# Performance work log

Measured on AMD Instinct MI355X. Metric: run time of the kernel, lower is better.

The kernel has to match this reference:

```python
import jax, jax.numpy as jnp
import numpy as np
import math

N_USER = 50000
N_ITEM = 50000
E_PER = 400000
F_IN = 128
F_OUT = 128
H = 4
D = F_OUT // H  # 32
NUM_ET = 2  # edge types: 0 = user->item, 1 = item->user


def setup_inputs() -> dict:
    key = jax.random.key(0)
    ks = jax.random.split(key, 16)
    s = 0.05  # weight scale to keep activations tame
    return {
        "x_user": jax.random.normal(ks[0], (N_USER, F_IN), jnp.float32),
        "x_item": jax.random.normal(ks[1], (N_ITEM, F_IN), jnp.float32),
        "W_kqv_user": jax.random.normal(ks[2], (F_IN, 3 * F_OUT), jnp.float32) * s,
        "b_kqv_user": jax.random.normal(ks[3], (3 * F_OUT,), jnp.float32) * s,
        "W_kqv_item": jax.random.normal(ks[4], (F_IN, 3 * F_OUT), jnp.float32) * s,
        "b_kqv_item": jax.random.normal(ks[5], (3 * F_OUT,), jnp.float32) * s,
        "Wk_rel": jax.random.normal(ks[6], (H * NUM_ET, D, D), jnp.float32) * s,
        "Wv_rel": jax.random.normal(ks[7], (H * NUM_ET, D, D), jnp.float32) * s,
        "W_out_user": jax.random.normal(ks[8], (F_OUT, F_OUT), jnp.float32) * s,
        "b_out_user": jax.random.normal(ks[9], (F_OUT,), jnp.float32) * s,
        "W_out_item": jax.random.normal(ks[10], (F_OUT, F_OUT), jnp.float32) * s,
        "b_out_item": jax.random.normal(ks[11], (F_OUT,), jnp.float32) * s,
        "skip_user": jnp.ones((1,), jnp.float32),
        "skip_item": jnp.ones((1,), jnp.float32),
        "p_rel_ui": jnp.ones((H,), jnp.float32),
        "p_rel_iu": jnp.ones((H,), jnp.float32),
        "edge_ui": jax.random.randint(ks[12], (2, E_PER), 0, N_USER, dtype=jnp.int32),
        "edge_iu": jax.random.randint(ks[13], (2, E_PER), 0, N_ITEM, dtype=jnp.int32),
    }


def _kqv(x, W, b):
    o = x @ W + b  # [N, 3F]
    k, q, v = o[:, :F_OUT], o[:, F_OUT:2 * F_OUT], o[:, 2 * F_OUT:]
    return (k.reshape(-1, H, D), q.reshape(-1, H, D), v.reshape(-1, H, D))


def _rel(x, Wrel, et):
    # HeteroLinear with type index h*NUM_ET + et per head (is_sorted layout)
    W = Wrel[jnp.arange(H) * NUM_ET + et]  # [H, D, D]
    return jnp.einsum('nhd,hde->nhe', x, W)


def reference(x_user, x_item, W_kqv_user, b_kqv_user, W_kqv_item, b_kqv_item,
              Wk_rel, Wv_rel, W_out_user, b_out_user, W_out_item, b_out_item,
              skip_user, skip_item, p_rel_ui, p_rel_iu, edge_ui, edge_iu):
    ku, qu, vu = _kqv(x_user, W_kqv_user, b_kqv_user)
    ki, qi, vi = _kqv(x_item, W_kqv_item, b_kqv_item)

    # per-edge-type relation transform of K/V (grouped GEMM by head x edge-type)
    k0, v0 = _rel(ku, Wk_rel, 0), _rel(vu, Wv_rel, 0)  # src of user->item
    k1, v1 = _rel(ki, Wk_rel, 1), _rel(vi, Wv_rel, 1)  # src of item->user

    q_all = jnp.concatenate([qu, qi], 0)  # dst offsets: user=0, item=N_USER
    n_tot = N_USER + N_ITEM

    src0, dst0 = edge_ui[0], edge_ui[1] + N_USER
    src1, dst1 = edge_iu[0], edge_iu[1]

    kj = jnp.concatenate([k0[src0], k1[src1]], 0)  # [E, H, D]
    vj = jnp.concatenate([v0[src0], v1[src1]], 0)  # [E, H, D]
    dst = jnp.concatenate([dst0, dst1], 0)         # [E]
    p = jnp.concatenate([jnp.broadcast_to(p_rel_ui, (E_PER, H)),
                         jnp.broadcast_to(p_rel_iu, (E_PER, H))], 0)

    qe = q_all[dst]                                  # [E, H, D]
    alpha = (qe * kj).sum(-1) * p / math.sqrt(D)     # [E, H]

    # segment softmax over destination nodes (PyG softmax: max-shift, +1e-16)
    amax = jax.ops.segment_max(alpha, dst, num_segments=n_tot)
    a = jnp.exp(alpha - amax[dst])
    denom = jax.ops.segment_sum(a, dst, num_segments=n_tot)
    a = a / (denom[dst] + 1e-16)

    out = jax.ops.segment_sum(vj * a[:, :, None], dst, num_segments=n_tot)
    out = out.reshape(n_tot, F_OUT)
    out_u, out_i = out[:N_USER], out[N_USER:]

    g = lambda t: jax.nn.gelu(t, approximate=False)
    a_u = g(out_u) @ W_out_user + b_out_user
    a_i = g(out_i) @ W_out_item + b_out_item

    su = jax.nn.sigmoid(skip_user)  # out_channels == in_channels -> skip blend
    si = jax.nn.sigmoid(skip_item)
    return (su * a_u + (1.0 - su) * x_user,
            si * a_i + (1.0 - si) * x_item)
```

## Files before the change

### kernel.cpp

```cpp
#include <hip/hip_runtime.h>
#include <hip/hip_bf16.h>
#include <math.h>

#define N_USERS 50000
#define N_ITEMS 50000
#define NN      100000
#define E_PER_  400000
#define E_TOT   800000
#define FDIM    128
#define NH      4
#define HD      32
#define SCAN_CHUNK 1024
#define SCAN_NB    ((NN + SCAN_CHUNK - 1) / SCAN_CHUNK)
#define KQV_NB  ((N_USERS + 127) / 128)

typedef __attribute__((ext_vector_type(8))) short bfrag;
typedef __attribute__((ext_vector_type(4))) float f32x4;

__device__ __forceinline__ float gelu_exact(float x) {
    return 0.5f * x * (1.0f + erff(x * 0.70710678118654752f));
}
__device__ __forceinline__ unsigned short f2bf(float f) {
    unsigned u = __float_as_uint(f);
    unsigned r = u + 0x7fffu + ((u >> 16) & 1u);
    return (unsigned short)(r >> 16);
}
__device__ __forceinline__ void unpack8(uint4 u, float* f) {
    f[0] = __uint_as_float(u.x << 16); f[1] = __uint_as_float(u.x & 0xffff0000u);
    f[2] = __uint_as_float(u.y << 16); f[3] = __uint_as_float(u.y & 0xffff0000u);
    f[4] = __uint_as_float(u.z << 16); f[5] = __uint_as_float(u.z & 0xffff0000u);
    f[6] = __uint_as_float(u.w << 16); f[7] = __uint_as_float(u.w & 0xffff0000u);
}
__device__ __forceinline__ size_t wfrag_idx(int n, int k) {
    int ch = n >> 7, nt = (n >> 4) & 7, lr = n & 15;
    int ks = k >> 5, lg = (k >> 3) & 3, e = k & 7;
    return ((size_t)(((ch * 8 + nt) * 4 + ks) * 64 + lg * 16 + lr)) * 8 + e;
}

__global__ void prep_kqv(
    const float* __restrict__ W_u, const float* __restrict__ b_u,
    const float* __restrict__ W_i, const float* __restrict__ b_i,
    const float* __restrict__ Wk_rel, const float* __restrict__ Wv_rel,
    unsigned short* __restrict__ F_u, float* __restrict__ bias_u,
    unsigned short* __restrict__ F_i, float* __restrict__ bias_i)
{
    const int et = blockIdx.x >= 384;
    const int n = blockIdx.x - et * 384;
    const int k = threadIdx.x;
    const float* W = et ? W_i : W_u;
    const float* b = et ? b_i : b_u;
    unsigned short* F = et ? F_i : F_u;
    float* bias_f = et ? bias_i : bias_u;
    float s;
    if (n < 128) {
        int h = n >> 5, e = n & 31;
        const float* wr = Wk_rel + (size_t)(h * 2 + et) * 1024 + e;
        const float* wc = W + (size_t)k * 384 + h * 32;
        s = 0.f;
        for (int d = 0; d < 32; ++d) s = fmaf(wc[d], wr[d * 32], s);
        if (k == 0) {
            float bs = 0.f;
            for (int d = 0; d < 32; ++d) bs = fmaf(b[h * 32 + d], wr[d * 32], bs);
            bias_f[n] = bs;
        }
    } else if (n < 256) {
        s = W[(size_t)k * 384 + n];
        if (k == 0) bias_f[n] = b[n];
    } else {
        int h = (n - 256) >> 5, e = (n - 256) & 31;
        const float* wr = Wv_rel + (size_t)(h * 2 + et) * 1024 + e;
        const float* wc = W + (size_t)k * 384 + 256 + h * 32;
        s = 0.f;
        for (int d = 0; d < 32; ++d) s = fmaf(wc[d], wr[d * 32], s);
        if (k == 0) {
            float bs = 0.f;
            for (int d = 0; d < 32; ++d) bs = fmaf(b[256 + h * 32 + d], wr[d * 32], bs);
            bias_f[n] = bs;
        }
    }
    F[wfrag_idx(n, k)] = f2bf(s);
}

__global__ void prep_wo(
    const float* __restrict__ W_u, unsigned short* __restrict__ F_u,
    const float* __restrict__ W_i, unsigned short* __restrict__ F_i)
{
    int i = blockIdx.x * blockDim.x + threadIdx.x;
    int side = i >= 128 * 128;
    int j = i - side * 128 * 128;
    if (j >= 128 * 128) return;
    int n = j >> 7, k = j & 127;
    const float* W = side ? W_i : W_u;
    unsigned short* F = side ? F_i : F_u;
    F[wfrag_idx(n, k)] = f2bf(W[(size_t)k * 128 + n]);
}

__global__ __launch_bounds__(256, 3) void kqv_mfma(
    const float* __restrict__ X_u, const unsigned short* __restrict__ F_u,
    const float* __restrict__ bias_u,
    const float* __restrict__ X_i, const unsigned short* __restrict__ F_i,
    const float* __restrict__ bias_i,
    unsigned short* __restrict__ kk_b,
    unsigned short* __restrict__ q_b,
    unsigned short* __restrict__ vv_b)
{
    const int t = threadIdx.x;
    const int side = blockIdx.x >= KQV_NB;
    const int m0 = (blockIdx.x - side * KQV_NB) * 128;
    const float* X = side ? X_i : X_u;
    const unsigned short* F = side ? F_i : F_u;
    const float* bias = side ? bias_i : bias_u;
    const int side_off = side ? N_USERS : 0;
    const int M = N_USERS;

    const int wave = t >> 6, lane = t & 63;
    const int lr = lane & 15, lg = lane >> 4;
    const int rbase = m0 + wave * 32;

    bfrag am[2][4];
    #pragma unroll
    for (int mt = 0; mt < 2; ++mt)
        #pragma unroll
        for (int ks = 0; ks < 4; ++ks) {
            int row = rbase + mt * 16 + lr;
            float4 a = make_float4(0.f, 0.f, 0.f, 0.f);
            float4 b4 = make_float4(0.f, 0.f, 0.f, 0.f);
            if (row < M) {
                const float* px = X + (size_t)row * 128 + ks * 32 + lg * 8;
                a  = *reinterpret_cast<const float4*>(px);
                b4 = *reinterpret_cast<const float4*>(px + 4);
            }
            uint4 pk;
            pk.x = (unsigned)f2bf(a.x)  | ((unsigned)f2bf(a.y)  << 16);
            pk.y = (unsigned)f2bf(a.z)  | ((unsigned)f2bf(a.w)  << 16);
            pk.z = (unsigned)f2bf(b4.x) | ((unsigned)f2bf(b4.y) << 16);
            pk.w = (unsigned)f2bf(b4.z) | ((unsigned)f2bf(b4.w) << 16);
            am[mt][ks] = *reinterpret_cast<bfrag*>(&pk);
        }

    #pragma unroll
    for (int ch = 0; ch < 3; ++ch) {
        f32x4 acc[2][8];
        const f32x4 zero = {0.f, 0.f, 0.f, 0.f};
        #pragma unroll
        for (int mt = 0; mt < 2; ++mt)
            #pragma unroll
            for (int nt = 0; nt < 8; ++nt) acc[mt][nt] = zero;

        bfrag bc[4], bn[4];
        #pragma unroll
        for (int ks = 0; ks < 4; ++ks)
            bc[ks] = *reinterpret_cast<const bfrag*>(
                F + ((size_t)((ch * 8 + 0) * 4 + ks) * 64 + lane) * 8);

        #pragma unroll
        for (int nt = 0; nt < 8; ++nt) {
            if (nt < 7) {
                #pragma unroll
                for (int ks = 0; ks < 4; ++ks)
                    bn[ks] = *reinterpret_cast<const bfrag*>(
                        F + ((size_t)((ch * 8 + nt + 1) * 4 + ks) * 64 + lane) * 8);
            }
            #pragma unroll
            for (int mt = 0; mt < 2; ++mt)
                #pragma unroll
                for (int ks = 0; ks < 4; ++ks)
                    acc[mt][nt] = __builtin_amdgcn_mfma_f32_16x16x32_bf16(
                        bc[ks], am[mt][ks], acc[mt][nt], 0, 0, 0);
            #pragma unroll
            for (int ks = 0; ks < 4; ++ks) bc[ks] = bn[ks];
        }

        unsigned short* arr = (ch == 0) ? kk_b : (ch == 1) ? q_b : vv_b;
        #pragma unroll
        for (int nt = 0; nt < 8; ++nt) {
            float4 bv = *reinterpret_cast<const float4*>(bias + ch * 128 + nt * 16 + lg * 4);
            #pragma unroll
            for (int mt = 0; mt < 2; ++mt) {
                int row = rbase + mt * 16 + lr;
                if (row < M) {
                    unsigned lo = (unsigned)f2bf(acc[mt][nt][0] + bv.x)
                                | ((unsigned)f2bf(acc[mt][nt][1] + bv.y) << 16);
                    unsigned hi = (unsigned)f2bf(acc[mt][nt][2] + bv.z)
                                | ((unsigned)f2bf(acc[mt][nt][3] + bv.w) << 16);
                    uint2 st = make_uint2(lo, hi);
                    *reinterpret_cast<uint2*>(
                        arr + (size_t)(side_off + row) * 128 + nt * 16 + lg * 4) = st;
                }
            }
        }
    }
}

__device__ __forceinline__ void edge_src_dst(
    int e, const int* __restrict__ edge_ui, const int* __restrict__ edge_iu,
    int& src, int& dst)
{
    if (e < E_PER_) {
        src = edge_ui[e];
        dst = edge_ui[E_PER_ + e] + N_USERS;
    } else {
        int e2 = e - E_PER_;
        src = N_USERS + edge_iu[e2];
        dst = edge_iu[E_PER_ + e2];
    }
}

__global__ __launch_bounds__(256) void hist_kernel(
    const int* __restrict__ edge_ui, const int* __restrict__ edge_iu,
    int* __restrict__ cnt)
{
    int e = blockIdx.x * blockDim.x + threadIdx.x;
    if (e >= E_TOT) return;
    int src, dst;
    edge_src_dst(e, edge_ui, edge_iu, src, dst);
    atomicAdd(cnt + dst, 1);
}

__global__ __launch_bounds__(256) void scan1_kernel(
    const int* __restrict__ cnt, int* __restrict__ base, int* __restrict__ bsum)
{
    __shared__ int ssum[256];
    const int t = threadIdx.x;
    const int i0 = blockIdx.x * SCAN_CHUNK + t * 4;
    int v[4];
    #pragma unroll
    for (int j = 0; j < 4; ++j) v[j] = (i0 + j < NN) ? cnt[i0 + j] : 0;
    int tsum = v[0] + v[1] + v[2] + v[3];
    ssum[t] = tsum;
    __syncthreads();
    int run = tsum;
    for (int off = 1; off < 256; off <<= 1) {
        int o = (t >= off) ? ssum[t - off] : 0;
        __syncthreads();
        run += o;
        ssum[t] = run;
        __syncthreads();
    }
    int excl = run - tsum;
    int p = excl;
    #pragma unroll
    for (int j = 0; j < 4; ++j) {
        if (i0 + j < NN) base[i0 + j] = p;
        p += v[j];
    }
    if (t == 255) bsum[blockIdx.x] = run;
}

__global__ __launch_bounds__(256) void scan3_kernel(
    int* __restrict__ base, const int* __restrict__ bsum, int* __restrict__ cursor)
{
    const int lane = threadIdx.x & 63;
    const int chunk = blockIdx.x >> 2;
    int v0 = (lane < chunk) ? bsum[lane] : 0;
    int v1 = (64 + lane < chunk && 64 + lane < SCAN_NB) ? bsum[64 + lane] : 0;
    int s = v0 + v1;
    #pragma unroll
    for (int off = 1; off < 64; off <<= 1) s += __shfl_xor(s, off);
    int i = blockIdx.x * 256 + threadIdx.x;
    if (i < NN) {
        int b = base[i] + s;
        base[i] = b;
        cursor[i] = b;
    }
}

__global__ __launch_bounds__(256) void fill_kernel(
    const int* __restrict__ edge_ui, const int* __restrict__ edge_iu,
    int* __restrict__ cursor, int* __restrict__ esrc)
{
    int e = blockIdx.x * blockDim.x + threadIdx.x;
    if (e >= E_TOT) return;
    int src, dst;
    edge_src_dst(e, edge_ui, edge_iu, src, dst);
    int pos = atomicAdd(cursor + dst, 1);
    esrc[pos] = src;
}

__global__ __launch_bounds__(256) void attn_fused(
    const unsigned short* __restrict__ q_b, const unsigned short* __restrict__ kk_b,
    const unsigned short* __restrict__ vv_b,
    const int* __restrict__ base, const int* __restrict__ cnt,
    const int* __restrict__ esrc,
    const float* __restrict__ p_ui, const float* __restrict__ p_iu,
    unsigned short* __restrict__ oa)
{
    const int wid  = (blockIdx.x * blockDim.x + threadIdx.x) >> 6;
    const int lane = threadIdx.x & 63;
    const int nw   = (gridDim.x * blockDim.x) >> 6;
    const int g    = lane >> 3;
    const int p    = lane & 7;
    const int h    = p >> 1;
    const float rsd = 0.17677669529663687f;
    const float pu = p_ui[h], pi = p_iu[h];

    for (int n = wid; n < NN; n += nw) {
        const float pr = (n >= N_USERS) ? pu : pi;
        float qf[16];
        {
            const unsigned short* qrow = q_b + (size_t)n * 128 + p * 16;
            unpack8(*reinterpret_cast<const uint4*>(qrow), qf);
            unpack8(*reinterpret_cast<const uint4*>(qrow + 8), qf + 8);
        }
        float l = 0.f;
        float acc[16];
        #pragma unroll
        for (int i = 0; i < 16; ++i) acc[i] = 0.f;
        const int s0 = base[n], c = cnt[n];

        for (int j = 0; j < c; j += 8) {
            int jj = j + g;
            bool valid = jj < c;
            int src = esrc[s0 + (valid ? jj : 0)];
            const unsigned short* krow = kk_b + (size_t)src * 128 + p * 16;
            const unsigned short* vrow = vv_b + (size_t)src * 128 + p * 16;
            uint4 k4a = *reinterpret_cast<const uint4*>(krow);
            uint4 k4b = *reinterpret_cast<const uint4*>(krow + 8);
            uint4 v4a = *reinterpret_cast<const uint4*>(vrow);
            uint4 v4b = *reinterpret_cast<const uint4*>(vrow + 8);
            float kf[16];
            unpack8(k4a, kf); unpack8(k4b, kf + 8);
            float s = qf[0] * kf[0];
            #pragma unroll
            for (int i = 1; i < 16; ++i) s = fmaf(qf[i], kf[i], s);
            s += __shfl_xor(s, 1);
            float w = valid ? __expf(s * pr * rsd) : 0.f;
            l += w;
            float vf[16];
            unpack8(v4a, vf); unpack8(v4b, vf + 8);
            #pragma unroll
            for (int i = 0; i < 16; ++i) acc[i] = fmaf(w, vf[i], acc[i]);
        }

        l += __shfl_xor(l, 8); l += __shfl_xor(l, 16); l += __shfl_xor(l, 32);

        const bool b2 = (g & 4) != 0;
        float k8[8];
        #pragma unroll
        for (int i = 0; i < 8; ++i) {
            float mine = b2 ? acc[8 + i] : acc[i];
            float send = b2 ? acc[i] : acc[8 + i];
            k8[i] = mine + __shfl_xor(send, 32);
        }
        const bool b1 = (g & 2) != 0;
        float k4r[4];
        #pragma unroll
        for (int i = 0; i < 4; ++i) {
            float mine = b1 ? k8[4 + i] : k8[i];
            float send = b1 ? k8[i] : k8[4 + i];
            k4r[i] = mine + __shfl_xor(send, 16);
        }
        const bool b0 = (g & 1) != 0;
        float k2[2];
        #pragma unroll
        for (int i = 0; i < 2; ++i) {
            float mine = b0 ? k4r[2 + i] : k4r[i];
            float send = b0 ? k4r[i] : k4r[2 + i];
            k2[i] = mine + __shfl_xor(send, 8);
        }
        float inv = 1.0f / (l + 1e-16f);
        unsigned pk = (unsigned)f2bf(gelu_exact(k2[0] * inv))
                    | ((unsigned)f2bf(gelu_exact(k2[1] * inv)) << 16);
        *reinterpret_cast<unsigned*>(oa + (size_t)n * 128 + p * 16 + 2 * g) = pk;
    }
}

__global__ __launch_bounds__(256, 3) void final_mfma(
    const unsigned short* __restrict__ oa,
    const float* __restrict__ x_u, const unsigned short* __restrict__ F_u,
    const float* __restrict__ bo_u, const float* __restrict__ skip_u,
    const float* __restrict__ x_i, const unsigned short* __restrict__ F_i,
    const float* __restrict__ bo_i, const float* __restrict__ skip_i,
    float* __restrict__ out)
{
    const int t = threadIdx.x;
    const int side = blockIdx.x >= KQV_NB;
    const int m0 = (blockIdx.x - side * KQV_NB) * 128;
    const float* x = side ? x_i : x_u;
    const unsigned short* F = side ? F_i : F_u;
    const float* bo = side ? bo_i : bo_u;
    const float* skip = side ? skip_i : skip_u;
    const int row_off = side ? N_USERS : 0;
    const int M = N_USERS;

    const int wave = t >> 6, lane = t & 63;
    const int lr = lane & 15, lg = lane >> 4;
    const int rbase = m0 + wave * 32;

    bfrag am[2][4];
    const bfrag bz = {0, 0, 0, 0, 0, 0, 0, 0};
    #pragma unroll
    for (int mt = 0; mt < 2; ++mt)
        #pragma unroll
        for (int ks = 0; ks < 4; ++ks) {
            int row = rbase + mt * 16 + lr;
            am[mt][ks] = (row < M)
                ? *reinterpret_cast<const bfrag*>(
                      oa + (size_t)(row_off + row) * 128 + ks * 32 + lg * 8)
                : bz;
        }

    f32x4 acc[2][8];
    const f32x4 zero = {0.f, 0.f, 0.f, 0.f};
    #pragma unroll
    for (int mt = 0; mt < 2; ++mt)
        #pragma unroll
        for (int nt = 0; nt < 8; ++nt) acc[mt][nt] = zero;

    bfrag bc[4], bn[4];
    #pragma unroll
    for (int ks = 0; ks < 4; ++ks)
        bc[ks] = *reinterpret_cast<const bfrag*>(
            F + ((size_t)(0 * 4 + ks) * 64 + lane) * 8);

    #pragma unroll
    for (int nt = 0; nt < 8; ++nt) {
        if (nt < 7) {
            #pragma unroll
            for (int ks = 0; ks < 4; ++ks)
                bn[ks] = *reinterpret_cast<const bfrag*>(
                    F + ((size_t)((nt + 1) * 4 + ks) * 64 + lane) * 8);
        }
        #pragma unroll
        for (int mt = 0; mt < 2; ++mt)
            #pragma unroll
            for (int ks = 0; ks < 4; ++ks)
                acc[mt][nt] = __builtin_amdgcn_mfma_f32_16x16x32_bf16(
                    bc[ks], am[mt][ks], acc[mt][nt], 0, 0, 0);
        #pragma unroll
        for (int ks = 0; ks < 4; ++ks) bc[ks] = bn[ks];
    }

    const float sg = 1.0f / (1.0f + expf(-skip[0]));
    #pragma unroll
    for (int nt = 0; nt < 8; ++nt) {
        float4 bv = *reinterpret_cast<const float4*>(bo + nt * 16 + lg * 4);
        #pragma unroll
        for (int mt = 0; mt < 2; ++mt) {
            int row = rbase + mt * 16 + lr;
            if (row < M) {
                float4 xv = *reinterpret_cast<const float4*>(
                    x + (size_t)row * 128 + nt * 16 + lg * 4);
                float4 res;
                res.x = sg * (acc[mt][nt][0] + bv.x) + (1.f - sg) * xv.x;
                res.y = sg * (acc[mt][nt][1] + bv.y) + (1.f - sg) * xv.y;
                res.z = sg * (acc[mt][nt][2] + bv.z) + (1.f - sg) * xv.z;
                res.w = sg * (acc[mt][nt][3] + bv.w) + (1.f - sg) * xv.w;
                *reinterpret_cast<float4*>(
                    out + (size_t)(row_off + row) * 128 + nt * 16 + lg * 4) = res;
            }
        }
    }
}

extern "C" void kernel_launch(void* const* d_in, const int* in_sizes, int n_in,
                              void* d_out, int out_size, void* d_ws, size_t ws_size,
                              hipStream_t stream)
{
    const float* x_user     = (const float*)d_in[0];
    const float* x_item     = (const float*)d_in[1];
    const float* W_kqv_user = (const float*)d_in[2];
    const float* b_kqv_user = (const float*)d_in[3];
    const float* W_kqv_item = (const float*)d_in[4];
    const float* b_kqv_item = (const float*)d_in[5];
    const float* Wk_rel     = (const float*)d_in[6];
    const float* Wv_rel     = (const float*)d_in[7];
    const float* W_out_user = (const float*)d_in[8];
    const float* b_out_user = (const float*)d_in[9];
    const float* W_out_item = (const float*)d_in[10];
    const float* b_out_item = (const float*)d_in[11];
    const float* skip_user  = (const float*)d_in[12];
    const float* skip_item  = (const float*)d_in[13];
    const float* p_ui       = (const float*)d_in[14];
    const float* p_iu       = (const float*)d_in[15];
    const int*   edge_ui    = (const int*)d_in[16];
    const int*   edge_iu    = (const int*)d_in[17];

    const size_t NODE_F = (size_t)NN * FDIM;
    char* w = (char*)d_ws;
    size_t off = 0;
    auto alloc = [&](size_t bytes) {
        char* p = w + off;
        off += (bytes + 255) & ~(size_t)255;
        return p;
    };
    unsigned short* q_b   = (unsigned short*)alloc(NODE_F * 2);
    unsigned short* kk_b  = (unsigned short*)alloc(NODE_F * 2);
    unsigned short* vv_b  = (unsigned short*)alloc(NODE_F * 2);
    unsigned short* oa_b  = (unsigned short*)alloc(NODE_F * 2);
    int* esrc   = (int*)alloc((size_t)E_TOT * 4);
    int* cnt    = (int*)alloc((size_t)NN * 4);
    int* base   = (int*)alloc((size_t)NN * 4);
    int* cursor = (int*)alloc((size_t)NN * 4);
    int* bsum   = (int*)alloc((size_t)SCAN_NB * 4);
    unsigned short* F_u    = (unsigned short*)alloc(384 * 128 * 2);
    unsigned short* F_i    = (unsigned short*)alloc(384 * 128 * 2);
    float*          bias_u = (float*)alloc(384 * 4);
    float*          bias_i = (float*)alloc(384 * 4);
    unsigned short* Fo_u   = (unsigned short*)alloc(128 * 128 * 2);
    unsigned short* Fo_i   = (unsigned short*)alloc(128 * 128 * 2);

    prep_kqv<<<768, 128, 0, stream>>>(W_kqv_user, b_kqv_user, W_kqv_item, b_kqv_item,
                                      Wk_rel, Wv_rel, F_u, bias_u, F_i, bias_i);
    prep_wo<<<128, 256, 0, stream>>>(W_out_user, Fo_u, W_out_item, Fo_i);

    kqv_mfma<<<2 * KQV_NB, 256, 0, stream>>>(x_user, F_u, bias_u,
                                             x_item, F_i, bias_i,
                                             kk_b, q_b, vv_b);

    hipMemsetAsync(cnt, 0, (size_t)NN * 4, stream);
    hist_kernel<<<(E_TOT + 255) / 256, 256, 0, stream>>>(edge_ui, edge_iu, cnt);
    scan1_kernel<<<SCAN_NB, 256, 0, stream>>>(cnt, base, bsum);
    scan3_kernel<<<(NN + 255) / 256, 256, 0, stream>>>(base, bsum, cursor);
    fill_kernel<<<(E_TOT + 255) / 256, 256, 0, stream>>>(edge_ui, edge_iu, cursor, esrc);

    attn_fused<<<2048, 256, 0, stream>>>(q_b, kk_b, vv_b, base, cnt, esrc,
                                         p_ui, p_iu, oa_b);

    final_mfma<<<2 * KQV_NB, 256, 0, stream>>>(
        oa_b, x_user, Fo_u, b_out_user, skip_user,
        x_item, Fo_i, b_out_item, skip_item, (float*)d_out);
}
```

Before: 244.6 us.

## Software-pipeline attention gather across nodes and pack base/count into int2

The attention kernel now prefetches the next node's query, metadata, first edge indices and first K/V rows while computing the current node, and issues the second edge group's loads up front. This hides the dependent index→row gather latency chain. Scan3 also writes a packed int2 (base, count) so each node needs a single metadata load. The cost is much higher register pressure from the staged uint4 buffers, which may reduce occupancy.

```diff
diff --git a/kernel.cpp b/kernel.cpp
--- a/kernel.cpp
+++ b/kernel.cpp
@@ -248,7 +248,9 @@
 }
 
 __global__ __launch_bounds__(256) void scan3_kernel(
-    int* __restrict__ base, const int* __restrict__ bsum, int* __restrict__ cursor)
+    const int* __restrict__ base, const int* __restrict__ bsum,
+    const int* __restrict__ cnt,
+    int* __restrict__ cursor, int2* __restrict__ meta2)
 {
     const int lane = threadIdx.x & 63;
     const int chunk = blockIdx.x >> 2;
@@ -260,8 +262,8 @@
     int i = blockIdx.x * 256 + threadIdx.x;
     if (i < NN) {
         int b = base[i] + s;
-        base[i] = b;
         cursor[i] = b;
+        meta2[i] = make_int2(b, cnt[i]);
     }
 }
 
@@ -280,8 +282,7 @@
 __global__ __launch_bounds__(256) void attn_fused(
     const unsigned short* __restrict__ q_b, const unsigned short* __restrict__ kk_b,
     const unsigned short* __restrict__ vv_b,
-    const int* __restrict__ base, const int* __restrict__ cnt,
-    const int* __restrict__ esrc,
+    const int2* __restrict__ meta2, const int* __restrict__ esrc,
     const float* __restrict__ p_ui, const float* __restrict__ p_iu,
     unsigned short* __restrict__ oa)
 {
@@ -293,41 +294,101 @@
     const int h    = p >> 1;
     const float rsd = 0.17677669529663687f;
     const float pu = p_ui[h], pi = p_iu[h];
-
-    for (int n = wid; n < NN; n += nw) {
+    const int EC = E_TOT - 1;
+
+    if (wid >= NN) return;
+
+    #define QA(nn)  (*reinterpret_cast<const uint4*>(q_b  + (size_t)(nn) * 128 + p * 16))
+    #define QB(nn)  (*reinterpret_cast<const uint4*>(q_b  + (size_t)(nn) * 128 + p * 16 + 8))
+    #define KA(ee)  (*reinterpret_cast<const uint4*>(kk_b + (size_t)(ee) * 128 + p * 16))
+    #define KB(ee)  (*reinterpret_cast<const uint4*>(kk_b + (size_t)(ee) * 128 + p * 16 + 8))
+    #define VA(ee)  (*reinterpret_cast<const uint4*>(vv_b + (size_t)(ee) * 128 + p * 16))
+    #define VB(ee)  (*reinterpret_cast<const uint4*>(vv_b + (size_t)(ee) * 128 + p * 16 + 8))
+
+    int n = wid;
+    int2 mtA = meta2[n];
+    uint4 qAa = QA(n), qAb = QB(n);
+    int sA = mtA.x, cA = mtA.y;
+    int j0A = (g < cA) ? g : 0;
+    int e0A = esrc[min(sA + j0A, EC)];
+    int e1A = esrc[min(sA + ((8 + g < cA) ? (8 + g) : j0A), EC)];
+    uint4 kAa = KA(e0A), kAb = KB(e0A), vAa = VA(e0A), vAb = VB(e0A);
+
+    int nB = n + nw;
+    bool hasB = nB < NN;
+    int sB = 0, cB = 0, e1B = 0;
+    uint4 qBa{}, qBb{}, kBa{}, kBb{}, vBa{}, vBb{};
+    if (hasB) {
+        int2 mtB = meta2[nB];
+        qBa = QA(nB); qBb = QB(nB);
+        sB = mtB.x; cB = mtB.y;
+        int j0 = (g < cB) ? g : 0;
+        int e0B = esrc[min(sB + j0, EC)];
+        e1B = esrc[min(sB + ((8 + g < cB) ? (8 + g) : j0), EC)];
+        kBa = KA(e0B); kBb = KB(e0B); vBa = VA(e0B); vBb = VB(e0B);
+    }
+
+    for (;;) {
+        const int nC = nB + nw;
+        const bool hasC = hasB && (nC < NN);
+        int2 mtC; uint4 qCa, qCb;
+        if (hasC) { mtC = meta2[nC]; qCa = QA(nC); qCb = QB(nC); }
+
+        const bool has2 = cA > 8;
+        uint4 k2a, k2b, v2a, v2b;
+        if (has2) { k2a = KA(e1A); k2b = KB(e1A); v2a = VA(e1A); v2b = VB(e1A); }
+
         const float pr = (n >= N_USERS) ? pu : pi;
         float qf[16];
-        {
-            const unsigned short* qrow = q_b + (size_t)n * 128 + p * 16;
-            unpack8(*reinterpret_cast<const uint4*>(qrow), qf);
-            unpack8(*reinterpret_cast<const uint4*>(qrow + 8), qf + 8);
-        }
+        unpack8(qAa, qf); unpack8(qAb, qf + 8);
         float l = 0.f;
         float acc[16];
         #pragma unroll
         for (int i = 0; i < 16; ++i) acc[i] = 0.f;
-        const int s0 = base[n], c = cnt[n];
-
-        for (int j = 0; j < c; j += 8) {
-            int jj = j + g;
-            bool valid = jj < c;
-            int src = esrc[s0 + (valid ? jj : 0)];
-            const unsigned short* krow = kk_b + (size_t)src * 128 + p * 16;
-            const unsigned short* vrow = vv_b + (size_t)src * 128 + p * 16;
-            uint4 k4a = *reinterpret_cast<const uint4*>(krow);
-            uint4 k4b = *reinterpret_cast<const uint4*>(krow + 8);
-            uint4 v4a = *reinterpret_cast<const uint4*>(vrow);
-            uint4 v4b = *reinterpret_cast<const uint4*>(vrow + 8);
+
+        {
             float kf[16];
-            unpack8(k4a, kf); unpack8(k4b, kf + 8);
+            unpack8(kAa, kf); unpack8(kAb, kf + 8);
             float s = qf[0] * kf[0];
             #pragma unroll
             for (int i = 1; i < 16; ++i) s = fmaf(qf[i], kf[i], s);
             s += __shfl_xor(s, 1);
-            float w = valid ? __expf(s * pr * rsd) : 0.f;
+            float w = (g < cA) ? __expf(s * pr * rsd) : 0.f;
             l += w;
             float vf[16];
-            unpack8(v4a, vf); unpack8(v4b, vf + 8);
+            unpack8(vAa, vf); unpack8(vAb, vf + 8);
+            #pragma unroll
+            for (int i = 0; i < 16; ++i) acc[i] = fmaf(w, vf[i], acc[i]);
+        }
+        if (has2) {
+            float kf[16];
+            unpack8(k2a, kf); unpack8(k2b, kf + 8);
+            float s = qf[0] * kf[0];
+            #pragma unroll
+            for (int i = 1; i < 16; ++i) s = fmaf(qf[i], kf[i], s);
+            s += __shfl_xor(s, 1);
+            float w = (8 + g < cA) ? __expf(s * pr * rsd) : 0.f;
+            l += w;
+            float vf[16];
+            unpack8(v2a, vf); unpack8(v2b, vf + 8);
+            #pragma unroll
+            for (int i = 0; i < 16; ++i) acc[i] = fmaf(w, vf[i], acc[i]);
+        }
+        for (int j = 16; j < cA; j += 8) {
+            int jj = j + g;
+            bool val = jj < cA;
+            int e = esrc[sA + (val ? jj : 0)];
+            uint4 ka = KA(e), kb = KB(e), va = VA(e), vb = VB(e);
+            float kf[16];
+            unpack8(ka, kf); unpack8(kb, kf + 8);
+            float s = qf[0] * kf[0];
+            #pragma unroll
+            for (int i = 1; i < 16; ++i) s = fmaf(qf[i], kf[i], s);
+            s += __shfl_xor(s, 1);
+            float w = val ? __expf(s * pr * rsd) : 0.f;
+            l += w;
+            float vf[16];
+            unpack8(va, vf); unpack8(vb, vf + 8);
             #pragma unroll
             for (int i = 0; i < 16; ++i) acc[i] = fmaf(w, vf[i], acc[i]);
         }
@@ -351,18 +412,40 @@
             k4r[i] = mine + __shfl_xor(send, 16);
         }
         const bool b0 = (g & 1) != 0;
-        float k2[2];
+        float k2r[2];
         #pragma unroll
         for (int i = 0; i < 2; ++i) {
             float mine = b0 ? k4r[2 + i] : k4r[i];
             float send = b0 ? k4r[i] : k4r[2 + i];
-            k2[i] = mine + __shfl_xor(send, 8);
+            k2r[i] = mine + __shfl_xor(send, 8);
         }
         float inv = 1.0f / (l + 1e-16f);
-        unsigned pk = (unsigned)f2bf(gelu_exact(k2[0] * inv))
-                    | ((unsigned)f2bf(gelu_exact(k2[1] * inv)) << 16);
+        unsigned pk = (unsigned)f2bf(gelu_exact(k2r[0] * inv))
+                    | ((unsigned)f2bf(gelu_exact(k2r[1] * inv)) << 16);
         *reinterpret_cast<unsigned*>(oa + (size_t)n * 128 + p * 16 + 2 * g) = pk;
-    }
+
+        if (!hasB) break;
+
+        n = nB;
+        sA = sB; cA = cB; e1A = e1B;
+        qAa = qBa; qAb = qBb;
+        kAa = kBa; kAb = kBb; vAa = vBa; vAb = vBb;
+        nB = nC; hasB = hasC;
+        if (hasC) {
+            qBa = qCa; qBb = qCb;
+            sB = mtC.x; cB = mtC.y;
+            int j0 = (g < cB) ? g : 0;
+            int e0B = esrc[min(sB + j0, EC)];
+            e1B = esrc[min(sB + ((8 + g < cB) ? (8 + g) : j0), EC)];
+            kBa = KA(e0B); kBb = KB(e0B); vBa = VA(e0B); vBb = VB(e0B);
+        }
+    }
+    #undef QA
+    #undef QB
+    #undef KA
+    #undef KB
+    #undef VA
+    #undef VB
 }
 
 __global__ __launch_bounds__(256, 3) void final_mfma(
@@ -493,6 +576,7 @@
     int* base   = (int*)alloc((size_t)NN * 4);
     int* cursor = (int*)alloc((size_t)NN * 4);
     int* bsum   = (int*)alloc((size_t)SCAN_NB * 4);
+    int2* meta2 = (int2*)alloc((size_t)NN * 8);
     unsigned short* F_u    = (unsigned short*)alloc(384 * 128 * 2);
     unsigned short* F_i    = (unsigned short*)alloc(384 * 128 * 2);
     float*          bias_u = (float*)alloc(384 * 4);
@@ -511,10 +595,10 @@
     hipMemsetAsync(cnt, 0, (size_t)NN * 4, stream);
     hist_kernel<<<(E_TOT + 255) / 256, 256, 0, stream>>>(edge_ui, edge_iu, cnt);
     scan1_kernel<<<SCAN_NB, 256, 0, stream>>>(cnt, base, bsum);
-    scan3_kernel<<<(NN + 255) / 256, 256, 0, stream>>>(base, bsum, cursor);
+    scan3_kernel<<<(NN + 255) / 256, 256, 0, stream>>>(base, bsum, cnt, cursor, meta2);
     fill_kernel<<<(E_TOT + 255) / 256, 256, 0, stream>>>(edge_ui, edge_iu, cursor, esrc);
 
-    attn_fused<<<2048, 256, 0, stream>>>(q_b, kk_b, vv_b, base, cnt, esrc,
+    attn_fused<<<2048, 256, 0, stream>>>(q_b, kk_b, vv_b, meta2, esrc,
                                          p_ui, p_iu, oa_b);
 
     final_mfma<<<2 * KQV_NB, 256, 0, stream>>>(
```

Measured after the change: 250.1 us. +2.2%, slower.
